# Performance work log

Measured on AMD Instinct MI355X. Metric: run time of the kernel, lower is better.

The kernel has to match this reference:

```python
import jax, jax.numpy as jnp
import numpy as np
import math

B, S, D, H = 64, 512, 768, 12
HS = D // H  # head size = 64


def setup_inputs() -> dict:
    key = jax.random.key(0)
    ks = jax.random.split(key, 8)
    scale = 1.0 / math.sqrt(D)
    return {
        "from_tensor": jax.random.normal(ks[0], (B, S, D), jnp.float32),
        "to_tensor": jax.random.normal(ks[1], (B, S, D), jnp.float32),
        "Wq": jax.random.normal(ks[2], (D, D), jnp.float32) * scale,
        "bq": jax.random.normal(ks[3], (D,), jnp.float32) * 0.02,
        "Wk": jax.random.normal(ks[4], (D, D), jnp.float32) * scale,
        "bk": jax.random.normal(ks[5], (D,), jnp.float32) * 0.02,
        "Wv": jax.random.normal(ks[6], (D, D), jnp.float32) * scale,
        "bv": jax.random.normal(ks[7], (D,), jnp.float32) * 0.02,
    }


def _split_heads(x):
    # [B, S, D] -> [B, H, S, HS]
    return x.reshape(B, S, H, HS).transpose(0, 2, 1, 3)


def reference(from_tensor, to_tensor, Wq, bq, Wk, bk, Wv, bv):
    q = _split_heads(from_tensor @ Wq + bq)
    k = _split_heads(to_tensor @ Wk + bk)
    v = _split_heads(to_tensor @ Wv + bv)
    scores = jnp.einsum("bhqd,bhkd->bhqk", q, k) / math.sqrt(HS)
    probs = jax.nn.softmax(scores, axis=-1)
    out = jnp.einsum("bhqk,bhkd->bhqd", probs, v)
    return out.transpose(0, 2, 1, 3).reshape(B, S, D)
```

## Files before the change

### kernel.cpp

```cpp
#include <hip/hip_runtime.h>
#include <hip/hip_bf16.h>

#define GAS __attribute__((address_space(1)))
#define LAS __attribute__((address_space(3)))

typedef __attribute__((ext_vector_type(8))) short   bf16x8;
typedef __attribute__((ext_vector_type(4))) float   f32x4;
typedef __attribute__((ext_vector_type(16))) float  f32x16;
typedef __attribute__((ext_vector_type(4))) float   f4;
typedef __attribute__((ext_vector_type(8))) short   s8v;
typedef __attribute__((ext_vector_type(2))) unsigned int u32x2;
typedef __attribute__((ext_vector_type(4))) unsigned int u32x4;

#define NB  64
#define NS  512
#define ND  768
#define NH  12
#define NHS 64
#define NM  (NB*NS)
#define NBH (NB*NH)

#define QSCALE 0.18033688011112042f

__device__ __forceinline__ unsigned short f2bf(float x){
  unsigned int u = __float_as_uint(x);
  u += 0x7fffu + ((u >> 16) & 1u);
  return (unsigned short)(u >> 16);
}

__device__ __forceinline__ f32x4 mfma16(bf16x8 a, bf16x8 b, f32x4 c){
  return __builtin_amdgcn_mfma_f32_16x16x32_bf16(a, b, c, 0, 0, 0);
}

__device__ __forceinline__ f32x16 mfma32(bf16x8 a, bf16x8 b, f32x16 c){
  return __builtin_amdgcn_mfma_f32_32x32x16_bf16(a, b, c, 0, 0, 0);
}

__device__ __forceinline__ unsigned int cvtpk(float lo, float hi){
  unsigned int r;
  asm("v_cvt_pk_bf16_f32 %0, %1, %2" : "=v"(r) : "v"(lo), "v"(hi));
  return r;
}

__device__ __forceinline__ bf16x8 u2b(u32x4 u){
  union { u32x4 a; bf16x8 b; } c; c.a = u; return c.b;
}

__global__ void cvt_x(const float* __restrict__ from_t, const float* __restrict__ to_t,
                      short* __restrict__ fb, short* __restrict__ tb){
  int v = blockIdx.x * 256 + threadIdx.x;
  const int NG = NM * ND / 8;
  const float* s; short* d;
  if (v < NG){ s = from_t; d = fb; } else { s = to_t; d = tb; v -= NG; }
  f4 a = ((const f4*)s)[(long)v * 2];
  f4 b = ((const f4*)s)[(long)v * 2 + 1];
  s8v o;
  o[0]=(short)f2bf(a[0]); o[1]=(short)f2bf(a[1]); o[2]=(short)f2bf(a[2]); o[3]=(short)f2bf(a[3]);
  o[4]=(short)f2bf(b[0]); o[5]=(short)f2bf(b[1]); o[6]=(short)f2bf(b[2]); o[7]=(short)f2bf(b[3]);
  ((s8v*)d)[v] = o;
}

__global__ void cvt_w(const float* __restrict__ Wq, const float* __restrict__ Wk,
                      const float* __restrict__ Wv, short* __restrict__ Wt){
  int i = blockIdx.x * 256 + threadIdx.x;
  int mat = i / (ND*ND);
  int rem = i - mat * (ND*ND);
  int k = rem / ND;
  int n = rem - k * ND;
  const float* W = (mat == 0) ? Wq : (mat == 1 ? Wk : Wv);
  Wt[(long)mat*ND*ND + (long)n*ND + k] = (short)f2bf(W[rem]);
}

__global__ __launch_bounds__(512, 2)
void qkv_gemm(const short* __restrict__ Xf, const short* __restrict__ Xt,
              const short* __restrict__ Wt,
              const float* __restrict__ bq, const float* __restrict__ bk,
              const float* __restrict__ bv,
              short* __restrict__ Qw, short* __restrict__ Kw, short* __restrict__ Vtw){
  __shared__ short smem[65536];

  int bid = blockIdx.x;
  int wg  = (bid & 7) * 144 + (bid >> 3);
  int mat = wg / 384;
  int r   = wg - mat * 384;
  int mt  = r / 3;
  int nt  = r - mt * 3;

  const short* A  = (mat == 0) ? Xf : Xt;
  const short* Wp = Wt + (long)mat * ND * ND;

  int t_ = threadIdx.x, wv = t_ >> 6, l = t_ & 63, g = l >> 4, c = l & 15;
  int wm = wv >> 2, wn = wv & 3;
  int m0 = mt * 256, n0 = nt * 256;

  auto stageH = [&](int kt2, int hf){
    int sl = kt2 & 3;
    short* base = smem + (hf ? 32768 : 0) + sl * 8192;
    const short* src = hf ? Wp : A;
    int r0 = hf ? n0 : m0;
    #pragma unroll
    for (int j = 0; j < 2; ++j){
      int idx = j * 512 + t_;
      int row = idx >> 2, slot = idx & 3;
      const short* gp = src + (long)(r0 + row) * ND + kt2 * 32 + ((slot ^ ((row >> 1) & 3)) << 3);
      __builtin_amdgcn_global_load_lds((const GAS unsigned int*)gp,
                                       (LAS unsigned int*)(base + idx * 8), 16, 0, 0);
    }
  };

  f32x4 zero = {0.f, 0.f, 0.f, 0.f};
  f32x4 acc[8][4];
  #pragma unroll
  for (int i = 0; i < 8; ++i)
    #pragma unroll
    for (int j = 0; j < 4; ++j) acc[i][j] = zero;

  stageH(0, 0); stageH(0, 1);
  stageH(1, 0); stageH(1, 1);
  stageH(2, 0); stageH(2, 1);
  asm volatile("s_waitcnt vmcnt(8)" ::: "memory");
  __builtin_amdgcn_s_barrier();

  bf16x8 bfr[4];
  for (int kt = 0; kt < 24; ++kt){
    int sl = kt & 3;
    const short* Asl = smem + sl * 8192;
    const short* Bsl = smem + 32768 + sl * 8192;

    bf16x8 af[4];
    #pragma unroll
    for (int i = 0; i < 4; ++i){
      int row = wm * 128 + i * 16 + c;
      af[i] = *(const bf16x8*)(Asl + row * 32 + ((g ^ ((row >> 1) & 3)) << 3));
    }
    #pragma unroll
    for (int ns = 0; ns < 4; ++ns){
      int row = wn * 64 + ns * 16 + c;
      bfr[ns] = *(const bf16x8*)(Bsl + row * 32 + ((g ^ ((row >> 1) & 3)) << 3));
    }
    if (kt < 21) stageH(kt + 3, 0);
    __builtin_amdgcn_s_barrier();
    asm volatile("s_waitcnt lgkmcnt(0)" ::: "memory");
    __builtin_amdgcn_sched_barrier(0);
    __builtin_amdgcn_s_setprio(1);
    #pragma unroll
    for (int i = 0; i < 4; ++i)
      #pragma unroll
      for (int ns = 0; ns < 4; ++ns)
        acc[i][ns] = mfma16(af[i], bfr[ns], acc[i][ns]);
    __builtin_amdgcn_s_setprio(0);
    __builtin_amdgcn_s_barrier();

    #pragma unroll
    for (int i = 0; i < 4; ++i){
      int row = wm * 128 + (4 + i) * 16 + c;
      af[i] = *(const bf16x8*)(Asl + row * 32 + ((g ^ ((row >> 1) & 3)) << 3));
    }
    if (kt < 21) stageH(kt + 3, 1);
    __builtin_amdgcn_s_barrier();
    asm volatile("s_waitcnt lgkmcnt(0)" ::: "memory");
    __builtin_amdgcn_sched_barrier(0);
    __builtin_amdgcn_s_setprio(1);
    #pragma unroll
    for (int i = 0; i < 4; ++i)
      #pragma unroll
      for (int ns = 0; ns < 4; ++ns)
        acc[4 + i][ns] = mfma16(af[i], bfr[ns], acc[4 + i][ns]);
    __builtin_amdgcn_s_setprio(0);
    if (kt <= 20)      asm volatile("s_waitcnt vmcnt(8)" ::: "memory");
    else if (kt == 21) asm volatile("s_waitcnt vmcnt(4)" ::: "memory");
    else if (kt == 22) asm volatile("s_waitcnt vmcnt(0)" ::: "memory");
    __builtin_amdgcn_s_barrier();
  }

  int n0g = n0 + wn * 64;
  const float* bias = (mat == 0) ? bq : (mat == 1 ? bk : bv);
  float bb[4];
  #pragma unroll
  for (int ns = 0; ns < 4; ++ns) bb[ns] = bias[n0g + ns * 16 + c];
  short* chunk = smem + wv * 4096;
  int hq = n0g >> 6;

  if (mat < 2){
    short* O = (mat == 0) ? Qw : Kw;
    float scl = (mat == 0) ? QSCALE : 1.0f;
    #pragma unroll
    for (int sp = 0; sp < 2; ++sp){
      #pragma unroll
      for (int msl = 0; msl < 4; ++msl){
        #pragma unroll
        for (int ns = 0; ns < 4; ++ns){
          int col = ns * 16 + c;
          #pragma unroll
          for (int i = 0; i < 4; ++i){
            int row = msl * 16 + g * 4 + i;
            chunk[row * 64 + (((col >> 3) ^ (row & 7)) << 3) + (col & 7)] =
                (short)f2bf((acc[sp * 4 + msl][ns][i] + bb[ns]) * scl);
          }
        }
      }
      asm volatile("s_waitcnt lgkmcnt(0)" ::: "memory");
      __builtin_amdgcn_sched_barrier(0);
      #pragma unroll
      for (int rr = 0; rr < 8; ++rr){
        int row = rr * 8 + (l >> 3);
        int slot = l & 7;
        bf16x8 v = *(const bf16x8*)(chunk + row * 64 + ((slot ^ (row & 7)) << 3));
        int m = m0 + wm * 128 + sp * 64 + row;
        int b = m >> 9, s2 = m & 511;
        *(bf16x8*)(O + (((long)(b * NH + hq) * NS + s2) << 6) + slot * 8) = v;
      }
      if (sp == 0){ asm volatile("s_waitcnt lgkmcnt(0)" ::: "memory"); }
    }
  } else {
    #pragma unroll
    for (int sp = 0; sp < 2; ++sp){
      #pragma unroll
      for (int msl = 0; msl < 4; ++msl){
        #pragma unroll
        for (int ns = 0; ns < 4; ++ns){
          int hs = ns * 16 + c;
          #pragma unroll
          for (int i = 0; i < 4; ++i){
            int col = msl * 16 + g * 4 + i;
            chunk[hs * 64 + (((col >> 3) ^ (hs & 7)) << 3) + (col & 7)] =
                (short)f2bf(acc[sp * 4 + msl][ns][i] + bb[ns]);
          }
        }
      }
      asm volatile("s_waitcnt lgkmcnt(0)" ::: "memory");
      __builtin_amdgcn_sched_barrier(0);
      int mbase = m0 + wm * 128 + sp * 64;
      int b = mbase >> 9, s0 = mbase & 511;
      #pragma unroll
      for (int rr = 0; rr < 8; ++rr){
        int hs = rr * 8 + (l >> 3);
        int slot = l & 7;
        bf16x8 v = *(const bf16x8*)(chunk + hs * 64 + ((slot ^ (hs & 7)) << 3));
        *(bf16x8*)(Vtw + (long)((b * NH + hq) * 64 + hs) * NS + s0 + slot * 8) = v;
      }
      if (sp == 0){ asm volatile("s_waitcnt lgkmcnt(0)" ::: "memory"); }
    }
  }
}

__global__ __launch_bounds__(512, 1)
void attn_kernel(const short* __restrict__ Qw, const short* __restrict__ Kw,
                 const short* __restrict__ Vtw, float* __restrict__ out){
  extern __shared__ char smem[];
  short* Ks = (short*)smem;
  short* Vs = (short*)(smem + 65536);

  int bh = blockIdx.x;
  int t = threadIdx.x, wv = t >> 6, l = t & 63;
  int lam = l & 31, hi = l >> 5;
  int r7 = lam & 7;

  const short* Kb = Kw  + (long)bh * NS * NHS;
  const short* Vb = Vtw + (long)bh * NS * NHS;

  #pragma unroll
  for (int it = 0; it < 8; ++it){
    int chunk = it * 8 + wv;
    {
      int idx = chunk * 64 + l;
      int row = idx >> 3, slot = idx & 7;
      const short* gk = Kb + row * 64 + ((slot ^ (row & 7)) * 8);
      __builtin_amdgcn_global_load_lds((const GAS unsigned int*)gk,
                                       (LAS unsigned int*)(Ks + chunk * 512), 16, 0, 0);
    }
    {
      int row = chunk, slot = l;
      const short* gv = Vb + (long)row * NS + (((slot & 56) | ((slot & 7) ^ (row & 7))) * 8);
      __builtin_amdgcn_global_load_lds((const GAS unsigned int*)gv,
                                       (LAS unsigned int*)(Vs + chunk * 512), 16, 0, 0);
    }
  }
  __syncthreads();

  int b = bh / NH, h = bh - b * NH;
  float* outb = out + (long)b * NS * ND + (long)h * 64;

  for (int qt = 0; qt < 2; ++qt){
    int q0 = wv * 64 + qt * 32;
    const short* Qb = Qw + (((long)bh * NS + q0 + lam) << 6) + hi * 8;
    bf16x8 qf[4];
    #pragma unroll
    for (int dk = 0; dk < 4; ++dk) qf[dk] = *(const bf16x8*)(Qb + dk * 16);

    f32x16 o0, o1;
    #pragma unroll
    for (int j = 0; j < 16; ++j){ o0[j] = 0.f; o1[j] = 0.f; }
    float m_run = -1e30f, lsum = 0.f;

    #pragma unroll
    for (int ch = 0; ch < 16; ++ch){
      f32x16 s;
      #pragma unroll
      for (int j = 0; j < 16; ++j) s[j] = 0.f;
      const char* kbase = (const char*)Ks + (ch * 32 + lam) * 128;
      #pragma unroll
      for (int dk = 0; dk < 4; ++dk){
        bf16x8 kf = *(const bf16x8*)(kbase + (((hi + 2 * dk) ^ r7) << 4));
        s = mfma32(kf, qf[dk], s);
      }

      float t8[8], t4[4];
      #pragma unroll
      for (int j = 0; j < 8; ++j) t8[j] = fmaxf(s[j], s[j + 8]);
      #pragma unroll
      for (int j = 0; j < 4; ++j) t4[j] = fmaxf(t8[j], t8[j + 4]);
      float m1 = fmaxf(fmaxf(t4[0], t4[1]), fmaxf(t4[2], t4[3]));
      float pmax = fmaxf(m1, __shfl_xor(m1, 32));
      if (__any(pmax > m_run + 8.0f)){
        float mnew = fmaxf(m_run, pmax);
        float cf = exp2f(m_run - mnew);
        lsum *= cf;
        #pragma unroll
        for (int j = 0; j < 16; ++j){ o0[j] *= cf; o1[j] *= cf; }
        m_run = mnew;
      }
      float p[16];
      #pragma unroll
      for (int j = 0; j < 16; ++j) p[j] = exp2f(s[j] - m_run);
      float a8[8], a4[4];
      #pragma unroll
      for (int j = 0; j < 8; ++j) a8[j] = p[j] + p[j + 8];
      #pragma unroll
      for (int j = 0; j < 4; ++j) a4[j] = a8[j] + a8[j + 4];
      lsum += (a4[0] + a4[1]) + (a4[2] + a4[3]);

      unsigned int w[8];
      #pragma unroll
      for (int rr = 0; rr < 8; ++rr) w[rr] = cvtpk(p[2 * rr], p[2 * rr + 1]);
      unsigned int y0 = (unsigned int)__shfl_xor((int)(hi ? w[0] : w[2]), 32);
      unsigned int y1 = (unsigned int)__shfl_xor((int)(hi ? w[1] : w[3]), 32);
      unsigned int y2 = (unsigned int)__shfl_xor((int)(hi ? w[4] : w[6]), 32);
      unsigned int y3 = (unsigned int)__shfl_xor((int)(hi ? w[5] : w[7]), 32);
      u32x4 fa, fb;
      if (hi){
        fa[0] = y0;   fa[1] = y1;   fa[2] = w[2]; fa[3] = w[3];
        fb[0] = y2;   fb[1] = y3;   fb[2] = w[6]; fb[3] = w[7];
      } else {
        fa[0] = w[0]; fa[1] = w[1]; fa[2] = y0;   fa[3] = y1;
        fb[0] = w[4]; fb[1] = w[5]; fb[2] = y2;   fb[3] = y3;
      }
      bf16x8 pa = u2b(fa), pb = u2b(fb);

      const char* vb0 = (const char*)Vs + lam * 1024;
      const char* vb1 = (const char*)Vs + (32 + lam) * 1024;
      int sl0 = ch * 4 + hi, sl1 = ch * 4 + 2 + hi;
      int sw0 = ((sl0 & 56) | ((sl0 & 7) ^ r7)) << 4;
      int sw1 = ((sl1 & 56) | ((sl1 & 7) ^ r7)) << 4;
      bf16x8 v00 = *(const bf16x8*)(vb0 + sw0);
      bf16x8 v01 = *(const bf16x8*)(vb0 + sw1);
      bf16x8 v10 = *(const bf16x8*)(vb1 + sw0);
      bf16x8 v11 = *(const bf16x8*)(vb1 + sw1);
      o0 = mfma32(v00, pa, o0);
      o0 = mfma32(v01, pb, o0);
      o1 = mfma32(v10, pa, o1);
      o1 = mfma32(v11, pb, o1);
    }

    float lt = lsum + __shfl_xor(lsum, 32);
    float invl = 1.0f / lt;
    float* orow = outb + (long)(q0 + lam) * ND;
    #pragma unroll
    for (int r = 0; r < 4; ++r){
      f4 u0, u1;
      #pragma unroll
      for (int jj = 0; jj < 4; ++jj){
        u0[jj] = o0[4 * r + jj] * invl;
        u1[jj] = o1[4 * r + jj] * invl;
      }
      *(f4*)(orow + 4 * hi + 8 * r)      = u0;
      *(f4*)(orow + 32 + 4 * hi + 8 * r) = u1;
    }
  }
}

extern "C" void kernel_launch(void* const* d_in, const int* in_sizes, int n_in,
                              void* d_out, int out_size, void* d_ws, size_t ws_size,
                              hipStream_t stream){
  const float* from_t = (const float*)d_in[0];
  const float* to_t   = (const float*)d_in[1];
  const float* Wq = (const float*)d_in[2];
  const float* bq = (const float*)d_in[3];
  const float* Wk = (const float*)d_in[4];
  const float* bk = (const float*)d_in[5];
  const float* Wv = (const float*)d_in[6];
  const float* bv = (const float*)d_in[7];

  short* fb  = (short*)d_ws;
  short* tb  = fb  + 25165824;
  short* Wt  = tb  + 25165824;
  short* Qw  = Wt  + 1769472;
  short* Kw  = Qw  + 25165824;
  short* Vtw = Kw  + 25165824;

  cvt_x<<<24576, 256, 0, stream>>>(from_t, to_t, fb, tb);
  cvt_w<<<6912, 256, 0, stream>>>(Wq, Wk, Wv, Wt);
  qkv_gemm<<<1152, 512, 0, stream>>>(fb, tb, Wt, bq, bk, bv, Qw, Kw, Vtw);
  attn_kernel<<<768, 512, 131072, stream>>>(Qw, Kw, Vtw, (float*)d_out);
}
```

Measured before the change: 330.2 us.

## Fuse fp32-to-bf16 activation conversion into QKV GEMM A-tile staging

Removes the separate cvt_x kernel and its bf16 copies of both activation tensors. The GEMM now loads fp32 activations into registers, converts them to bf16 with packed conversion, and writes them to swizzled LDS one stage later. B tiles still use direct global-to-LDS loads. This cuts a full read-write pass over about 200MB of activations, but each GEMM now reads twice the bytes for A (three n-tiles re-read fp32), uses more registers, and has a different wait-count schedule.

```diff
diff --git a/kernel.cpp b/kernel.cpp
--- a/kernel.cpp
+++ b/kernel.cpp
@@ -44,20 +44,6 @@
 
 __device__ __forceinline__ bf16x8 u2b(u32x4 u){
   union { u32x4 a; bf16x8 b; } c; c.a = u; return c.b;
-}
-
-__global__ void cvt_x(const float* __restrict__ from_t, const float* __restrict__ to_t,
-                      short* __restrict__ fb, short* __restrict__ tb){
-  int v = blockIdx.x * 256 + threadIdx.x;
-  const int NG = NM * ND / 8;
-  const float* s; short* d;
-  if (v < NG){ s = from_t; d = fb; } else { s = to_t; d = tb; v -= NG; }
-  f4 a = ((const f4*)s)[(long)v * 2];
-  f4 b = ((const f4*)s)[(long)v * 2 + 1];
-  s8v o;
-  o[0]=(short)f2bf(a[0]); o[1]=(short)f2bf(a[1]); o[2]=(short)f2bf(a[2]); o[3]=(short)f2bf(a[3]);
-  o[4]=(short)f2bf(b[0]); o[5]=(short)f2bf(b[1]); o[6]=(short)f2bf(b[2]); o[7]=(short)f2bf(b[3]);
-  ((s8v*)d)[v] = o;
 }
 
 __global__ void cvt_w(const float* __restrict__ Wq, const float* __restrict__ Wk,
@@ -72,7 +58,7 @@
 }
 
 __global__ __launch_bounds__(512, 2)
-void qkv_gemm(const short* __restrict__ Xf, const short* __restrict__ Xt,
+void qkv_gemm(const float* __restrict__ from_t, const float* __restrict__ to_t,
               const short* __restrict__ Wt,
               const float* __restrict__ bq, const float* __restrict__ bk,
               const float* __restrict__ bv,
@@ -86,23 +72,47 @@
   int mt  = r / 3;
   int nt  = r - mt * 3;
 
-  const short* A  = (mat == 0) ? Xf : Xt;
+  const float* Af = (mat == 0) ? from_t : to_t;
   const short* Wp = Wt + (long)mat * ND * ND;
 
   int t_ = threadIdx.x, wv = t_ >> 6, l = t_ & 63, g = l >> 4, c = l & 15;
   int wm = wv >> 2, wn = wv & 3;
   int m0 = mt * 256, n0 = nt * 256;
 
-  auto stageH = [&](int kt2, int hf){
-    int sl = kt2 & 3;
-    short* base = smem + (hf ? 32768 : 0) + sl * 8192;
-    const short* src = hf ? Wp : A;
-    int r0 = hf ? n0 : m0;
+  f4 areg[4];
+
+  auto stageA_load = [&](int kt2){
     #pragma unroll
     for (int j = 0; j < 2; ++j){
       int idx = j * 512 + t_;
       int row = idx >> 2, slot = idx & 3;
-      const short* gp = src + (long)(r0 + row) * ND + kt2 * 32 + ((slot ^ ((row >> 1) & 3)) << 3);
+      const float* gp = Af + (long)(m0 + row) * ND + kt2 * 32 + slot * 8;
+      areg[j * 2]     = *(const f4*)(gp);
+      areg[j * 2 + 1] = *(const f4*)(gp + 4);
+    }
+  };
+  auto stageA_write = [&](int kt2){
+    short* base = smem + (kt2 & 3) * 8192;
+    #pragma unroll
+    for (int j = 0; j < 2; ++j){
+      int idx = j * 512 + t_;
+      int row = idx >> 2, slot = idx & 3;
+      int sw = slot ^ ((row >> 1) & 3);
+      u32x4 pk;
+      pk[0] = cvtpk(areg[j * 2][0],     areg[j * 2][1]);
+      pk[1] = cvtpk(areg[j * 2][2],     areg[j * 2][3]);
+      pk[2] = cvtpk(areg[j * 2 + 1][0], areg[j * 2 + 1][1]);
+      pk[3] = cvtpk(areg[j * 2 + 1][2], areg[j * 2 + 1][3]);
+      *(bf16x8*)(base + row * 32 + sw * 8) = u2b(pk);
+    }
+  };
+  auto stageB = [&](int kt2){
+    short* base = smem + 32768 + (kt2 & 3) * 8192;
+    #pragma unroll
+    for (int j = 0; j < 2; ++j){
+      int idx = j * 512 + t_;
+      int row = idx >> 2, slot = idx & 3;
+      const short* gp = Wp + (long)(n0 + row) * ND + kt2 * 32 + ((slot ^ ((row >> 1) & 3)) << 3);
       __builtin_amdgcn_global_load_lds((const GAS unsigned int*)gp,
                                        (LAS unsigned int*)(base + idx * 8), 16, 0, 0);
     }
@@ -115,10 +125,15 @@
     #pragma unroll
     for (int j = 0; j < 4; ++j) acc[i][j] = zero;
 
-  stageH(0, 0); stageH(0, 1);
-  stageH(1, 0); stageH(1, 1);
-  stageH(2, 0); stageH(2, 1);
+  stageB(0);
+  stageA_load(0);
+  stageA_write(0);
+  stageA_load(1);
+  stageA_write(1);
+  stageA_load(2);
+  stageB(1); stageB(2);
   asm volatile("s_waitcnt vmcnt(8)" ::: "memory");
+  asm volatile("s_waitcnt lgkmcnt(0)" ::: "memory");
   __builtin_amdgcn_s_barrier();
 
   bf16x8 bfr[4];
@@ -138,7 +153,8 @@
       int row = wn * 64 + ns * 16 + c;
       bfr[ns] = *(const bf16x8*)(Bsl + row * 32 + ((g ^ ((row >> 1) & 3)) << 3));
     }
-    if (kt < 21) stageH(kt + 3, 0);
+    if (kt < 22) stageA_write(kt + 2);
+    if (kt < 21) stageA_load(kt + 3);
     __builtin_amdgcn_s_barrier();
     asm volatile("s_waitcnt lgkmcnt(0)" ::: "memory");
     __builtin_amdgcn_sched_barrier(0);
@@ -156,7 +172,7 @@
       int row = wm * 128 + (4 + i) * 16 + c;
       af[i] = *(const bf16x8*)(Asl + row * 32 + ((g ^ ((row >> 1) & 3)) << 3));
     }
-    if (kt < 21) stageH(kt + 3, 1);
+    if (kt < 21) stageB(kt + 3);
     __builtin_amdgcn_s_barrier();
     asm volatile("s_waitcnt lgkmcnt(0)" ::: "memory");
     __builtin_amdgcn_sched_barrier(0);
@@ -168,7 +184,7 @@
         acc[4 + i][ns] = mfma16(af[i], bfr[ns], acc[4 + i][ns]);
     __builtin_amdgcn_s_setprio(0);
     if (kt <= 20)      asm volatile("s_waitcnt vmcnt(8)" ::: "memory");
-    else if (kt == 21) asm volatile("s_waitcnt vmcnt(4)" ::: "memory");
+    else if (kt == 21) asm volatile("s_waitcnt vmcnt(2)" ::: "memory");
     else if (kt == 22) asm volatile("s_waitcnt vmcnt(0)" ::: "memory");
     __builtin_amdgcn_s_barrier();
   }
@@ -391,15 +407,12 @@
   const float* Wv = (const float*)d_in[6];
   const float* bv = (const float*)d_in[7];
 
-  short* fb  = (short*)d_ws;
-  short* tb  = fb  + 25165824;
-  short* Wt  = tb  + 25165824;
+  short* Wt  = (short*)d_ws;
   short* Qw  = Wt  + 1769472;
   short* Kw  = Qw  + 25165824;
   short* Vtw = Kw  + 25165824;
 
-  cvt_x<<<24576, 256, 0, stream>>>(from_t, to_t, fb, tb);
   cvt_w<<<6912, 256, 0, stream>>>(Wq, Wk, Wv, Wt);
-  qkv_gemm<<<1152, 512, 0, stream>>>(fb, tb, Wt, bq, bk, bv, Qw, Kw, Vtw);
+  qkv_gemm<<<1152, 512, 0, stream>>>(from_t, to_t, Wt, bq, bk, bv, Qw, Kw, Vtw);
   attn_kernel<<<768, 512, 131072, stream>>>(Qw, Kw, Vtw, (float*)d_out);
 }
```

New measurement: 312.2 us. 1.06x faster.
